# Optimization experiments

Hardware: AMD Instinct MI355X
Metric: run time of the kernel (lower is better)

Reference implementation:

```python
import jax, jax.numpy as jnp
import numpy as np

B, N = 1, 6
C, H, W = 256, 32, 88          # featureShape
ORH, ORW = 256, 704            # transformed image shape
OC = 128                       # out_channels
DV = jnp.arange(1.0, 45.0, 1.0)  # depth bin centers, d_conf=(1,45,1)
D = DV.shape[0]                # 44
BN_EPS = 1e-3


def _conv(x, w, b, pad):
    y = jax.lax.conv_general_dilated(x, w, (1, 1), [(pad, pad), (pad, pad)],
                                     dimension_numbers=("NCHW", "OIHW", "NCHW"))
    return y + b[None, :, None, None]


def _bn(x, g, be, m, v):
    scale = g / jnp.sqrt(v + BN_EPS)
    return (x - m[None, :, None, None]) * scale[None, :, None, None] + be[None, :, None, None]


def _frustum():
    ds = jnp.broadcast_to(DV[:, None, None], (D, H, W))
    xs = jnp.broadcast_to(jnp.linspace(0.0, ORW - 1.0, W)[None, None, :], (D, H, W))
    ys = jnp.broadcast_to(jnp.linspace(0.0, ORH - 1.0, H)[None, :, None], (D, H, W))
    return jnp.stack((xs, ys, ds), -1)  # (D,H,W,3)


def _forward(rot, trans, K, prot, ptrans, feats,
             w1, b1, g1, be1, m1, v1, w2, b2, g2, be2, m2, v2, w3, b3):
    # ---- geometry: undo image augmentation, unproject, map cam->ego ----
    fr = _frustum()
    pts = fr[None, None] - ptrans[:, :, None, None, None, :]              # (B,N,D,H,W,3)
    pts = jnp.einsum("bnij,bndhwj->bndhwi", jnp.linalg.inv(prot), pts)
    pts = jnp.concatenate((pts[..., :2] * pts[..., 2:3], pts[..., 2:3]), -1)
    combine = jnp.einsum("bnij,bnjk->bnik", rot, jnp.linalg.inv(K))
    geom = jnp.einsum("bnij,bndhwj->bndhwi", combine, pts) + trans[:, :, None, None, None, :]
    # ---- depth net (conv-bn-relu x2 + 1x1 head) ----
    x = feats.reshape(B * N, C, H, W)
    x = jax.nn.relu(_bn(_conv(x, w1, b1, 1), g1, be1, m1, v1))
    x = jax.nn.relu(_bn(_conv(x, w2, b2, 1), g2, be2, m2, v2))
    x = _conv(x, w3, b3, 0)                                              # (BN, OC+2, H, W)
    mu, log_sigma, f = x[:, 0], x[:, 1], x[:, 2:]
    sigma = jnp.exp(log_sigma) + 1e-6
    # per-pixel Gaussian over depth bins, normalized over D
    gauss = jnp.exp(-0.5 * (DV[None, :, None, None] - mu[:, None]) ** 2 / (sigma[:, None] ** 2))  # (BN,D,H,W)
    gauss = gauss / (gauss.sum(1, keepdims=True) + 1e-6)
    # outer product depth-dist x features -> (BN, OC, D, H, W)
    out = gauss[:, None] * f[:, :, None]
    out = out.reshape(B, N, OC, D, H, W).transpose(0, 1, 3, 4, 5, 2)     # (B,N,D,H,W,OC)
    return geom, out


def setup_inputs():
    key = jax.random.key(0)
    ks = jax.random.split(key, 9)
    eye = jnp.eye(3)
    rot = eye + 0.1 * jax.random.normal(ks[0], (B, N, 3, 3), jnp.float32)
    trans = jax.random.normal(ks[1], (B, N, 3), jnp.float32)
    Kbase = jnp.array([[600.0, 0.0, 352.0], [0.0, 600.0, 128.0], [0.0, 0.0, 1.0]])
    K = jnp.broadcast_to(Kbase, (B, N, 3, 3)) * (1.0 + 0.01 * jax.random.normal(ks[2], (B, N, 3, 3)))
    prot = eye + 0.05 * jax.random.normal(ks[3], (B, N, 3, 3), jnp.float32)
    ptrans = jax.random.normal(ks[4], (B, N, 3), jnp.float32)
    feats = 0.5 * jax.random.normal(ks[5], (B, N, C, H, W), jnp.float32)
    w1 = 0.02 * jax.random.normal(ks[6], (C, C, 3, 3), jnp.float32); b1 = jnp.zeros((C,))
    w2 = 0.02 * jax.random.normal(ks[7], (C, C, 3, 3), jnp.float32); b2 = jnp.zeros((C,))
    w3 = 0.02 * jax.random.normal(ks[8], (OC + 2, C, 1, 1), jnp.float32); b3 = jnp.zeros((OC + 2,))
    ones = jnp.ones((C,)); zeros = jnp.zeros((C,))
    return dict(cam2ego_rot=rot, cam2ego_trans=trans, cam_intrins=K,
                post_cam2ego_rot=prot, post_cam2ego_trans=ptrans, img_feats=feats,
                w1=w1, b1=b1, g1=ones, be1=zeros, m1=zeros, v1=ones,
                w2=w2, b2=b2, g2=ones, be2=zeros, m2=zeros, v2=ones,
                w3=w3, b3=b3)


def reference(cam2ego_rot, cam2ego_trans, cam_intrins, post_cam2ego_rot, post_cam2ego_trans, img_feats,
              w1, b1, g1, be1, m1, v1, w2, b2, g2, be2, m2, v2, w3, b3):
    return _forward(cam2ego_rot, cam2ego_trans, cam_intrins, post_cam2ego_rot, post_cam2ego_trans, img_feats,
                    w1, b1, g1, be1, m1, v1, w2, b2, g2, be2, m2, v2, w3, b3)
```

## Files before the change

kernel.cpp:

```cpp
#include <hip/hip_runtime.h>
#include <hip/hip_fp16.h>
#include <hip/hip_fp8.h>
#include <stdint.h>

typedef _Float16 f16;
typedef _Float16 half8 __attribute__((ext_vector_type(8)));
typedef _Float16 half4v __attribute__((ext_vector_type(4)));
typedef float floatx4 __attribute__((ext_vector_type(4)));
typedef long long i64;
typedef long long i64x2 __attribute__((ext_vector_type(2)));

#define NCAM 6
#define NPIX 16896
#define CIN 256
#define OUT1_OFF 2230272

#define AB_OFF     4096
#define W3P_OFF    16384
#define W1P_OFF    163840
#define W2P_OFF    1343488
#define XPAD_OFF   2523136
#define Y1P_OFF    11923456
#define XPAD8_BYTES 4700160
#define Y1P8_OFF   (XPAD_OFF + XPAD8_BYTES)
#define Y3_WS_OFF  21323776
#define Y3_BYTES   8921088

#define PIPE_BAR6()  asm volatile("s_waitcnt vmcnt(6) lgkmcnt(0)\n\ts_barrier" ::: "memory")
#define PIPE_BAR0()  asm volatile("s_waitcnt vmcnt(0) lgkmcnt(0)\n\ts_barrier" ::: "memory")
#define PIPE_BARL()  asm volatile("s_waitcnt lgkmcnt(0)\n\ts_barrier" ::: "memory")

__device__ __forceinline__ void gld16(const void* gsrc, void* ldst) {
    typedef __attribute__((address_space(1))) const uint32_t GBuf;
    typedef __attribute__((address_space(3))) uint32_t LBuf;
    __builtin_amdgcn_global_load_lds((GBuf*)(uintptr_t)gsrc,
                                     (LBuf*)(uint32_t)(uintptr_t)ldst,
                                     16, 0, 0);
}

__device__ __forceinline__ uint8_t f2fp8(float v) {
    __hip_fp8_e4m3 q(v);
    return (uint8_t)q.__x;
}

__device__ __forceinline__ int fp8pos(int c) {
    int c128 = c & 127;
    int P  = c128 >> 6;
    int kh = (c128 >> 5) & 1;
    int ks = (c128 >> 3) & 3;
    return (c >> 7) * 128 + (P * 4 + ks) * 16 + kh * 8 + (c & 7);
}

__device__ __forceinline__ void inv3(const float* m, float* o) {
    float a=m[0],b=m[1],c=m[2],d=m[3],e=m[4],f=m[5],g=m[6],h=m[7],i=m[8];
    float A  =  (e*i - f*h);
    float Bc = -(d*i - f*g);
    float Cc =  (d*h - e*g);
    float det = a*A + b*Bc + c*Cc;
    float r = 1.0f/det;
    o[0]=A*r;   o[1]=-(b*i - c*h)*r; o[2]= (b*f - c*e)*r;
    o[3]=Bc*r;  o[4]= (a*i - c*g)*r; o[5]=-(a*f - c*d)*r;
    o[6]=Cc*r;  o[7]=-(a*h - b*g)*r; o[8]= (a*e - b*d)*r;
}

__device__ __forceinline__ void geom_point(int idx,
        const float* __restrict__ rot, const float* __restrict__ trans,
        const float* __restrict__ K, const float* __restrict__ prot,
        const float* __restrict__ ptrans, float* __restrict__ out) {
    int w = idx % 88;
    int h = (idx / 88) % 32;
    int d = (idx / 2816) % 44;
    int n = idx / 123904;
    float P[9], Km[9], R[9], iP[9], iK[9], C[9];
    #pragma unroll
    for (int i = 0; i < 9; ++i) { P[i]=prot[n*9+i]; Km[i]=K[n*9+i]; R[i]=rot[n*9+i]; }
    inv3(P, iP);
    inv3(Km, iK);
    #pragma unroll
    for (int i = 0; i < 3; ++i)
        #pragma unroll
        for (int j = 0; j < 3; ++j)
            C[i*3+j] = R[i*3+0]*iK[0*3+j] + R[i*3+1]*iK[1*3+j] + R[i*3+2]*iK[2*3+j];
    float fx = w * (703.0f / 87.0f);
    float fy = h * (255.0f / 31.0f);
    float fz = d + 1.0f;
    float px = fx - ptrans[n*3+0], py = fy - ptrans[n*3+1], pz = fz - ptrans[n*3+2];
    float q0 = iP[0]*px + iP[1]*py + iP[2]*pz;
    float q1 = iP[3]*px + iP[4]*py + iP[5]*pz;
    float q2 = iP[6]*px + iP[7]*py + iP[8]*pz;
    float r0 = q0 * q2, r1 = q1 * q2, r2 = q2;
    out[idx*3 + 0] = C[0]*r0 + C[1]*r1 + C[2]*r2 + trans[n*3+0];
    out[idx*3 + 1] = C[3]*r0 + C[4]*r1 + C[5]*r2 + trans[n*3+1];
    out[idx*3 + 2] = C[6]*r0 + C[7]*r1 + C[8]*r2 + trans[n*3+2];
}

__global__ __launch_bounds__(256) void fused_prep(
        const float* __restrict__ rot, const float* __restrict__ trans,
        const float* __restrict__ K, const float* __restrict__ prot,
        const float* __restrict__ ptrans, const float* __restrict__ feats,
        const float* __restrict__ w1, const float* __restrict__ w2,
        const float* __restrict__ w3,
        const float* __restrict__ b1, const float* __restrict__ g1,
        const float* __restrict__ be1, const float* __restrict__ m1, const float* __restrict__ v1,
        const float* __restrict__ b2, const float* __restrict__ g2,
        const float* __restrict__ be2, const float* __restrict__ m2, const float* __restrict__ v2,
        const float* __restrict__ b3,
        uint8_t* __restrict__ w1p, uint8_t* __restrict__ w2p, f16* __restrict__ w3p,
        float* __restrict__ ab, uint8_t* __restrict__ xpad8, uint8_t* __restrict__ y1p8,
        float* __restrict__ geomOut) {
    int bid = blockIdx.x;
    int t = threadIdx.x;
    if (bid < 12) {
        uint8_t* buf = (bid < 6) ? xpad8 : y1p8;
        int n = bid % 6;
        for (int i = t; i < 3904; i += 256) {
            int u = i >> 4, c = i & 15;
            int h, w;
            if (u < 90)       { h = 0;       w = u; }
            else if (u < 180) { h = 33;      w = u - 90; }
            else if (u < 212) { h = u - 179; w = 0; }
            else              { h = u - 211; w = 89; }
            *(uint4*)&buf[((size_t)((n*34 + h)*90 + w))*256 + c*16] = uint4{0,0,0,0};
        }
        return;
    }
    if (bid < 716) {
        int oc = bid - 12;
        if (oc < 512) {
            const float* s = ((oc < 256) ? w1 : w2) + (size_t)(oc & 255) * 2304;
            uint8_t* dst = ((oc < 256) ? w1p : w2p) + (size_t)(oc & 255) * 2304;
            for (int idx = t; idx < 2304; idx += 256) {
                int win = idx >> 7, b = idx & 127;
                int sl = b >> 4, j = b & 15;
                int P = sl >> 2, ks = sl & 3, kh = j >> 3, jj = j & 7;
                int kwin = (2*P + kh)*32 + ks*8 + jj;
                int Kg = win*128 + kwin;
                int tap = Kg >> 8, c = Kg & 255;
                dst[idx] = f2fp8(s[c*9 + tap] * 16.0f);
            }
        } else {
            int r = oc - 512;
            w3p[r * 256 + t] = (r < 130) ? (f16)w3[r * 256 + t] : (f16)0.0f;
        }
        return;
    }
    if (bid < 1484) {
        __shared__ float tile[64][89];
        int b = bid - 716;
        int n = b >> 7;
        int h = (b >> 2) & 31;
        int icg = b & 3;
        int ic0 = icg * 64;
        #pragma unroll
        for (int j = 0; j < 22; ++j) {
            int idx = j * 256 + t;
            int r = idx / 88, w = idx - r * 88;
            tile[r][w] = feats[((size_t)(n*256 + ic0 + r) * 32 + h) * 88 + w];
        }
        __syncthreads();
        for (int j = 0; j < 6; ++j) {
            int idx = j * 256 + t;
            if (idx < 1408) {
                int w = idx >> 4, cq = idx & 15;
                int c = cq * 4;
                int ca = ic0 + c;
                uint32_t u = (uint32_t)f2fp8(tile[c][w])
                           | ((uint32_t)f2fp8(tile[c+1][w]) << 8)
                           | ((uint32_t)f2fp8(tile[c+2][w]) << 16)
                           | ((uint32_t)f2fp8(tile[c+3][w]) << 24);
                size_t px = (size_t)((n*34 + h + 1) * 90 + (w + 1));
                *(uint32_t*)&xpad8[px*256 + fp8pos(ca)] = u;
            }
        }
        return;
    }
    if (bid == 1484) {
        float a1 = g1[t] * rsqrtf(v1[t] + 1e-3f);
        ab[t]       = a1 * 0.0625f;
        ab[256 + t] = (b1[t] - m1[t]) * a1 + be1[t];
        float a2 = g2[t] * rsqrtf(v2[t] + 1e-3f);
        ab[512 + t] = a2 * 0.0625f;
        ab[768 + t] = (b2[t] - m2[t]) * a2 + be2[t];
        if (t < 192) ab[1024 + t] = (t < 130) ? b3[t] : 0.0f;
        return;
    }
    int idx = (bid - 1485) * 256 + t;
    geom_point(idx, rot, trans, K, prot, ptrans, geomOut);
}

__global__ void geom_k(const float* __restrict__ rot, const float* __restrict__ trans,
                       const float* __restrict__ K, const float* __restrict__ prot,
                       const float* __restrict__ ptrans, float* __restrict__ out) {
    int idx = blockIdx.x * 256 + threadIdx.x;
    geom_point(idx, rot, trans, K, prot, ptrans, out);
}

template<bool FP8OUT>
__global__ __launch_bounds__(256, 3) void conv8_mfma(
        const uint8_t* __restrict__ xin,
        const uint8_t* __restrict__ wp,
        const float* __restrict__ ab, int abOff,
        uint8_t* __restrict__ yout8,
        f16* __restrict__ yout16)
{
    __shared__ alignas(16) uint8_t Ald[2][64 * 128];
    __shared__ alignas(16) uint8_t Bld[2][128 * 128];
    int t = threadIdx.x;
    int l = t & 63;
    int wid = t >> 6;
    int bid = (blockIdx.x & 7) * 66 + (blockIdx.x >> 3);
    int bm = bid & 3;
    int bn = bid >> 2;
    int p0 = bn * 128;
    int wm = wid >> 1, wn = wid & 1;
    int swz = (l & 7) ^ (l >> 3);

    const uint8_t* asrc = wp + (size_t)(bm*64 + wid*16 + (l >> 3)) * 2304 + swz * 16;
    size_t bsrc[4];
    #pragma unroll
    for (int i = 0; i < 4; ++i) {
        int p = p0 + wid*32 + i*8 + (l >> 3);
        int n = p / 2816; int rem = p - n * 2816;
        int hh = rem / 88; int ww = rem - hh * 88;
        bsrc[i] = (size_t)((n*34 + hh) * 90 + ww) * 256 + swz * 16;
    }
    int aoff = wid * 2048 + l * 16;
    int boff = wid * 4096 + l * 16;

    floatx4 acc[2][4] = {};

    auto stage = [&](int win, uint8_t* Ab, uint8_t* Bb) {
        int tap = win >> 1;
        int koff = ((tap/3) * 90 + (tap%3)) * 256 + (win & 1) * 128;
        const uint8_t* aw = asrc + win * 128;
        gld16(aw,             Ab + aoff);
        gld16(aw + 8 * 2304,  Ab + aoff + 1024);
        #pragma unroll
        for (int j = 0; j < 4; ++j)
            gld16(xin + bsrc[j] + koff, Bb + boff + j * 1024);
    };
    auto compute = [&](const uint8_t* Ab, const uint8_t* Bb) {
        #pragma unroll
        for (int P = 0; P < 2; ++P) {
            i64x2 af[2], bf[4];
            int sl = (((P << 2) | (l >> 4)) ^ (l & 7)) * 16;
            #pragma unroll
            for (int m = 0; m < 2; ++m) {
                int row = wm*32 + m*16 + (l & 15);
                af[m] = *(const i64x2*)&Ab[row * 128 + sl];
            }
            #pragma unroll
            for (int n = 0; n < 4; ++n) {
                int row = wn*64 + n*16 + (l & 15);
                bf[n] = *(const i64x2*)&Bb[row * 128 + sl];
            }
            __builtin_amdgcn_s_setprio(1);
            #pragma unroll
            for (int m = 0; m < 2; ++m)
                #pragma unroll
                for (int n = 0; n < 4; ++n) {
                    acc[m][n] = __builtin_amdgcn_mfma_f32_16x16x32_fp8_fp8(af[m].x, bf[n].x, acc[m][n], 0, 0, 0);
                    acc[m][n] = __builtin_amdgcn_mfma_f32_16x16x32_fp8_fp8(af[m].y, bf[n].y, acc[m][n], 0, 0, 0);
                }
            __builtin_amdgcn_s_setprio(0);
        }
    };

    stage(0, Ald[0], Bld[0]);
    stage(1, Ald[1], Bld[1]);
    #pragma unroll 1
    for (int win = 0; win < 16; win += 2) {
        PIPE_BAR6(); compute(Ald[0], Bld[0]);
        PIPE_BARL(); stage(win + 2, Ald[0], Bld[0]);
        PIPE_BAR6(); compute(Ald[1], Bld[1]);
        PIPE_BARL(); stage(win + 3, Ald[1], Bld[1]);
    }
    PIPE_BAR6(); compute(Ald[0], Bld[0]);
    PIPE_BAR0(); compute(Ald[1], Bld[1]);

    int ocb = bm*64 + wm*32;
    #pragma unroll
    for (int m = 0; m < 2; ++m) {
        int oc0 = ocb + m*16 + (l >> 4) * 4;
        float4 av = *(const float4*)&ab[abOff + oc0];
        float4 bv = *(const float4*)&ab[abOff + 256 + oc0];
        #pragma unroll
        for (int n = 0; n < 4; ++n) {
            int p = p0 + wn*64 + n*16 + (l & 15);
            int ni = p / 2816; int rem = p - ni * 2816;
            int hh = rem / 88; int ww = rem - hh * 88;
            size_t pxb = (size_t)((ni*34 + hh + 1) * 90 + (ww + 1)) * 256;
            float v0 = fmaxf(fmaf(acc[m][n][0], av.x, bv.x), 0.0f);
            float v1 = fmaxf(fmaf(acc[m][n][1], av.y, bv.y), 0.0f);
            float v2 = fmaxf(fmaf(acc[m][n][2], av.z, bv.z), 0.0f);
            float v3 = fmaxf(fmaf(acc[m][n][3], av.w, bv.w), 0.0f);
            if (FP8OUT) {
                uint32_t u = (uint32_t)f2fp8(v0)
                           | ((uint32_t)f2fp8(v1) << 8)
                           | ((uint32_t)f2fp8(v2) << 16)
                           | ((uint32_t)f2fp8(v3) << 24);
                *(uint32_t*)&yout8[pxb + fp8pos(oc0)] = u;
            } else {
                half4v hv;
                hv[0] = (f16)v0; hv[1] = (f16)v1; hv[2] = (f16)v2; hv[3] = (f16)v3;
                *(half4v*)&yout16[pxb + oc0] = hv;
            }
        }
    }
}

__global__ __launch_bounds__(256) void conv3_mfma(
        const f16* __restrict__ xin,
        const f16* __restrict__ wp3,
        const float* __restrict__ b3p,
        float* __restrict__ y3)
{
    __shared__ alignas(16) f16 Ald[3][64 * 64];
    __shared__ alignas(16) f16 Bld[3][128 * 64];
    int t = threadIdx.x;
    int l = t & 63;
    int wid = t >> 6;
    int bm = blockIdx.x % 3;
    int bn = blockIdx.x / 3;
    int p0 = bn * 128;
    int wm = wid >> 1, wn = wid & 1;
    int swz = (l & 7) ^ (l >> 3);

    const f16* asrc = wp3 + (size_t)(bm*64 + wid*16 + (l >> 3)) * 256 + swz * 8;
    size_t bsrc[4];
    #pragma unroll
    for (int i = 0; i < 4; ++i) {
        int p = p0 + wid*32 + i*8 + (l >> 3);
        int n = p / 2816; int rem = p - n * 2816;
        int hh = rem / 88; int ww = rem - hh * 88;
        bsrc[i] = (size_t)((n*34 + hh) * 90 + ww) * 256 + swz * 8;
    }
    int aoff = wid * 16 * 64;
    int boff = wid * 32 * 64;

    floatx4 acc[2][4] = {};

    auto stage = [&](int kt, f16* Ab, f16* Bb) {
        int koff = (1 * 90 + 1) * 256 + kt * 64;
        int k0 = kt * 64;
        gld16(asrc + k0,            Ab + aoff);
        gld16(asrc + k0 + 8 * 256,  Ab + aoff + 8 * 64);
        gld16(xin + bsrc[0] + koff, Bb + boff);
        gld16(xin + bsrc[1] + koff, Bb + boff + 8 * 64);
        gld16(xin + bsrc[2] + koff, Bb + boff + 16 * 64);
        gld16(xin + bsrc[3] + koff, Bb + boff + 24 * 64);
    };
    auto compute = [&](const f16* Ab, const f16* Bb) {
        #pragma unroll
        for (int kk = 0; kk < 2; ++kk) {
            half8 af[2], bf[4];
            int kslot = kk * 4 + (l >> 4);
            #pragma unroll
            for (int m = 0; m < 2; ++m) {
                int row = wm*32 + m*16 + (l & 15);
                af[m] = *(const half8*)&Ab[row * 64 + ((kslot ^ (row & 7)) * 8)];
            }
            #pragma unroll
            for (int n = 0; n < 4; ++n) {
                int row = wn*64 + n*16 + (l & 15);
                bf[n] = *(const half8*)&Bb[row * 64 + ((kslot ^ (row & 7)) * 8)];
            }
            __builtin_amdgcn_s_setprio(1);
            #pragma unroll
            for (int m = 0; m < 2; ++m)
                #pragma unroll
                for (int n = 0; n < 4; ++n)
                    acc[m][n] = __builtin_amdgcn_mfma_f32_16x16x32_f16(af[m], bf[n], acc[m][n], 0, 0, 0);
            __builtin_amdgcn_s_setprio(0);
        }
    };

    stage(0, Ald[0], Bld[0]);
    stage(1, Ald[1], Bld[1]);
    PIPE_BAR6(); stage(2, Ald[2], Bld[2]); compute(Ald[0], Bld[0]);
    PIPE_BAR6(); stage(3, Ald[0], Bld[0]); compute(Ald[1], Bld[1]);
    PIPE_BAR6(); compute(Ald[2], Bld[2]);
    PIPE_BAR0(); compute(Ald[0], Bld[0]);

    int ocb = bm*64 + wm*32;
    #pragma unroll
    for (int m = 0; m < 2; ++m) {
        int oc0 = ocb + m*16 + (l >> 4) * 4;
        if (oc0 < 132) {
            float4 bv = *(const float4*)&b3p[oc0];
            #pragma unroll
            for (int n = 0; n < 4; ++n) {
                int p = p0 + wn*64 + n*16 + (l & 15);
                float4 v;
                v.x = acc[m][n][0] + bv.x;
                v.y = acc[m][n][1] + bv.y;
                v.z = acc[m][n][2] + bv.z;
                v.w = acc[m][n][3] + bv.w;
                *(float4*)&y3[(size_t)p * 132 + oc0] = v;
            }
        }
    }
}

__global__ __launch_bounds__(256) void splat_k(
        const float* __restrict__ y3,
        float* __restrict__ out)
{
    int t = threadIdx.x;
    int l = t & 63;
    int wid = t >> 6;
    int p = blockIdx.x * 4 + wid;
    int n = p / 2816; int rem = p - n * 2816;
    int h = rem / 88; int w = rem - h * 88;
    const float* row = y3 + (size_t)p * 132;

    float2 f2 = *(const float2*)&row[2 + 2*l];
    float mu = row[0];
    float ls = row[1];
    float sig = expf(ls) + 1e-6f;
    float g = 0.0f;
    if (l < 44) { float z = (l + 1.0f) - mu; g = expf(-0.5f * z * z / (sig * sig)); }
    float s = g;
    #pragma unroll
    for (int off = 32; off; off >>= 1) s += __shfl_down(s, off);
    s = __shfl(s, 0);
    float gn = g / (s + 1e-6f);

    size_t pxb = ((size_t)(n * 44) * 32 + h) * 88 + w;
    float* o1 = out + OUT1_OFF;
    #pragma unroll 4
    for (int d = 0; d < 44; ++d) {
        float gg = __shfl(gn, d);
        float2 v; v.x = gg * f2.x; v.y = gg * f2.y;
        *(float2*)&o1[(pxb + (size_t)d * 2816) * 128 + 2*l] = v;
    }
}

extern "C" void kernel_launch(void* const* d_in, const int* in_sizes, int n_in,
                              void* d_out, int out_size, void* d_ws, size_t ws_size,
                              hipStream_t stream) {
    const float* rot    = (const float*)d_in[0];
    const float* trans  = (const float*)d_in[1];
    const float* K      = (const float*)d_in[2];
    const float* prot   = (const float*)d_in[3];
    const float* ptrans = (const float*)d_in[4];
    const float* feats  = (const float*)d_in[5];
    const float* w1     = (const float*)d_in[6];
    const float* b1     = (const float*)d_in[7];
    const float* g1     = (const float*)d_in[8];
    const float* be1    = (const float*)d_in[9];
    const float* m1     = (const float*)d_in[10];
    const float* v1     = (const float*)d_in[11];
    const float* w2     = (const float*)d_in[12];
    const float* b2     = (const float*)d_in[13];
    const float* g2     = (const float*)d_in[14];
    const float* be2    = (const float*)d_in[15];
    const float* m2     = (const float*)d_in[16];
    const float* v2     = (const float*)d_in[17];
    const float* w3     = (const float*)d_in[18];
    const float* b3     = (const float*)d_in[19];

    char* ws = (char*)d_ws;
    float*   ab    = (float*)(ws + AB_OFF);
    f16*     w3p   = (f16*)(ws + W3P_OFF);
    uint8_t* w1p8  = (uint8_t*)(ws + W1P_OFF);
    uint8_t* w2p8  = (uint8_t*)(ws + W2P_OFF);
    uint8_t* xpad8 = (uint8_t*)(ws + XPAD_OFF);
    uint8_t* y1p8  = (uint8_t*)(ws + Y1P8_OFF);
    f16*     y2    = (f16*)(ws + Y1P_OFF);
    float*   out   = (float*)d_out;

    bool y3InWs = ws_size >= (size_t)(Y3_WS_OFF + Y3_BYTES);
    float* y3 = y3InWs ? (float*)(ws + Y3_WS_OFF) : out;
    int geomBlocks = y3InWs ? 2904 : 0;

    fused_prep<<<1485 + geomBlocks, 256, 0, stream>>>(
        rot, trans, K, prot, ptrans, feats, w1, w2, w3,
        b1, g1, be1, m1, v1, b2, g2, be2, m2, v2, b3,
        w1p8, w2p8, w3p, ab, xpad8, y1p8, out);
    conv8_mfma<true><<<528, 256, 0, stream>>>(xpad8, w1p8, ab, 0, y1p8, nullptr);
    conv8_mfma<false><<<528, 256, 0, stream>>>(y1p8, w2p8, ab, 512, nullptr, y2);
    conv3_mfma<<<396, 256, 0, stream>>>(y2, w3p, ab + 1024, y3);
    splat_k<<<4224, 256, 0, stream>>>(y3, out);
    if (!y3InWs)
        geom_k<<<2904, 256, 0, stream>>>(rot, trans, K, prot, ptrans, out);
}
```

Baseline: 140.2 us.

## Widen splat stores to float4 nontemporal and precompute gaussians in shared memory

The splat kernel now handles 8 pixels per block, with 32 lanes per pixel each writing 4 channels instead of 64 lanes writing 2. The depth gaussians and their normalisation are computed once into shared memory rather than by shuffle reductions. Output writes use 128-bit nontemporal stores so the large write-once output does not pollute cache. This targets store bandwidth in the output-dominated splat, at the cost of two block barriers and a serial 44-element sum done by 8 threads.

```diff
diff --git a/kernel.cpp b/kernel.cpp
--- a/kernel.cpp
+++ b/kernel.cpp
@@ -406,33 +406,46 @@
         const float* __restrict__ y3,
         float* __restrict__ out)
 {
+    __shared__ float eg[8][44];
+    __shared__ float rs[8];
     int t = threadIdx.x;
+    int p0 = blockIdx.x * 8;
+
+    for (int i = t; i < 352; i += 256) {
+        int px = i / 44, d = i - px * 44;
+        const float* row = y3 + (size_t)(p0 + px) * 132;
+        float mu = row[0];
+        float sig = expf(row[1]) + 1e-6f;
+        float z = (d + 1.0f) - mu;
+        eg[px][d] = expf(-0.5f * z * z / (sig * sig));
+    }
+    __syncthreads();
+    if (t < 8) {
+        float s = 0.0f;
+        for (int d = 0; d < 44; ++d) s += eg[t][d];
+        rs[t] = 1.0f / (s + 1e-6f);
+    }
+    __syncthreads();
+
     int l = t & 63;
     int wid = t >> 6;
-    int p = blockIdx.x * 4 + wid;
+    int px = wid * 2 + (l >> 5);
+    int ch = (l & 31) * 4;
+    int p = p0 + px;
     int n = p / 2816; int rem = p - n * 2816;
     int h = rem / 88; int w = rem - h * 88;
     const float* row = y3 + (size_t)p * 132;
-
-    float2 f2 = *(const float2*)&row[2 + 2*l];
-    float mu = row[0];
-    float ls = row[1];
-    float sig = expf(ls) + 1e-6f;
-    float g = 0.0f;
-    if (l < 44) { float z = (l + 1.0f) - mu; g = expf(-0.5f * z * z / (sig * sig)); }
-    float s = g;
-    #pragma unroll
-    for (int off = 32; off; off >>= 1) s += __shfl_down(s, off);
-    s = __shfl(s, 0);
-    float gn = g / (s + 1e-6f);
+    floatx4 f4 = *(const floatx4*)&row[2 + ch];
+    float rsv = rs[px];
 
     size_t pxb = ((size_t)(n * 44) * 32 + h) * 88 + w;
     float* o1 = out + OUT1_OFF;
     #pragma unroll 4
     for (int d = 0; d < 44; ++d) {
-        float gg = __shfl(gn, d);
-        float2 v; v.x = gg * f2.x; v.y = gg * f2.y;
-        *(float2*)&o1[(pxb + (size_t)d * 2816) * 128 + 2*l] = v;
+        float gg = eg[px][d] * rsv;
+        floatx4 v;
+        v.x = gg * f4.x; v.y = gg * f4.y; v.z = gg * f4.z; v.w = gg * f4.w;
+        __builtin_nontemporal_store(v, (floatx4*)&o1[(pxb + (size_t)d * 2816) * 128 + ch]);
     }
 }
 
@@ -481,7 +494,7 @@
     conv8_mfma<true><<<528, 256, 0, stream>>>(xpad8, w1p8, ab, 0, y1p8, nullptr);
     conv8_mfma<false><<<528, 256, 0, stream>>>(y1p8, w2p8, ab, 512, nullptr, y2);
     conv3_mfma<<<396, 256, 0, stream>>>(y2, w3p, ab + 1024, y3);
-    splat_k<<<4224, 256, 0, stream>>>(y3, out);
+    splat_k<<<2112, 256, 0, stream>>>(y3, out);
     if (!y3InWs)
         geom_k<<<2904, 256, 0, stream>>>(rot, trans, K, prot, ptrans, out);
 }
```

Measured after the change: 131.8 us. -6.0%, faster.
